# Kernel tuning notes

Hardware: AMD Instinct MI355X
Metric: run time of the kernel (lower is better)

The kernel has to match this reference:

```python
import jax, jax.numpy as jnp
import numpy as np

N = 50000          # num_nodes
E = 600000         # num_edges
D_IN = 128         # gcn_embed_dims[0]
D_H = 128          # gcn_embed_dims[1]
D_OUT = 64         # gcn_embed_dims[2]
D_MLP = 64         # mlp hidden


def setup_inputs() -> dict:
    key = jax.random.key(0)
    ks = jax.random.split(key, 10)
    s = lambda fan: 1.0 / np.sqrt(fan).astype(np.float32)
    return {
        "X": jax.random.normal(ks[0], (N, D_IN), jnp.float32),
        "edges": jax.random.randint(ks[1], (2, E), 0, N, dtype=jnp.int32),
        # GCN layer 1
        "Wg1": jax.random.normal(ks[2], (D_IN, D_H), jnp.float32) * s(D_IN),
        "bg1": jnp.zeros((D_H,), jnp.float32),
        # GCN layer 2
        "Wg2": jax.random.normal(ks[3], (D_H, D_OUT), jnp.float32) * s(D_H),
        "bg2": jnp.zeros((D_OUT,), jnp.float32),
        # decoder MLP: in = 2*D_OUT = 128
        "Wm1": jax.random.normal(ks[4], (2 * D_OUT, D_MLP), jnp.float32) * s(2 * D_OUT),
        "bm1": jnp.zeros((D_MLP,), jnp.float32),
        "Wm2": jax.random.normal(ks[5], (D_MLP, 1), jnp.float32) * s(D_MLP),
        "bm2": jnp.zeros((1,), jnp.float32),
    }


def gcn_conv(X, W, b, src, dst):
    """GCNConv: out = D^{-1/2} (A + I) D^{-1/2} X W + b (PyG semantics)."""
    n = X.shape[0]
    XW = X @ W                                   # [N, d_out]
    loop = jnp.arange(n, dtype=src.dtype)
    src2 = jnp.concatenate([src, loop])          # add self-loops
    dst2 = jnp.concatenate([dst, loop])
    deg = jax.ops.segment_sum(jnp.ones_like(dst2, dtype=XW.dtype), dst2,
                              num_segments=n)    # in-degree incl. self-loop
    dinv = jax.lax.rsqrt(jnp.maximum(deg, 1.0))  # deg >= 1 due to self-loop
    norm = dinv[src2] * dinv[dst2]               # [E+N]
    out = jax.ops.segment_sum(XW[src2] * norm[:, None], dst2, num_segments=n)
    return out + b


def reference(X, edges, Wg1, bg1, Wg2, bg2, Wm1, bm1, Wm2, bm2):
    src, dst = edges[0], edges[1]
    # encode: GCNConv -> ReLU -> GCNConv
    H = jax.nn.relu(gcn_conv(X, Wg1, bg1, src, dst))
    H = gcn_conv(H, Wg2, bg2, src, dst)          # [N, 64]
    # decode: gather endpoints, concat, MLP
    Z = jnp.concatenate([H[src], H[dst]], axis=-1)  # [E, 128]
    Z = jax.nn.relu(Z @ Wm1 + bm1)                   # [E, 64]
    return Z @ Wm2 + bm2                             # [E, 1]
```

## Files before the change

### kernel.cpp

```cpp
#include <hip/hip_runtime.h>


typedef __attribute__((ext_vector_type(8))) short bf8v;
typedef __attribute__((ext_vector_type(4))) float fa4v;

__device__ __forceinline__ ushort to_bf(float x) {
    unsigned u = __float_as_uint(x);
    unsigned r = (u + 0x7fffu + ((u >> 16) & 1u)) >> 16;
    return (ushort)r;
}
__device__ __forceinline__ float from_bf(ushort h) {
    return __uint_as_float(((unsigned)h) << 16);
}

__global__ void deg_count_k(const int* __restrict__ dst, int* __restrict__ cnt, int E) {
    int i = blockIdx.x * 256 + threadIdx.x;
    if (i < E) atomicAdd(&cnt[dst[i]], 1);
}

__global__ void deg_inv_k(const int* __restrict__ cnt, float* __restrict__ dinv, int n) {
    int i = blockIdx.x * 256 + threadIdx.x;
    if (i < n) dinv[i] = rsqrtf((float)cnt[i] + 1.0f);
}

__global__ void scan_a_k(const int* __restrict__ cnt, int* __restrict__ excl,
                         int* __restrict__ bsum, int n) {
    __shared__ int sd[256];
    int t = threadIdx.x;
    int base = blockIdx.x * 1024 + t * 4;
    int v0 = 0, v1 = 0, v2 = 0, v3 = 0;
    if (base + 0 < n) v0 = cnt[base + 0];
    if (base + 1 < n) v1 = cnt[base + 1];
    if (base + 2 < n) v2 = cnt[base + 2];
    if (base + 3 < n) v3 = cnt[base + 3];
    int sum = v0 + v1 + v2 + v3;
    int acc = sum;
    sd[t] = acc;
    __syncthreads();
    for (int off = 1; off < 256; off <<= 1) {
        int x = (t >= off) ? sd[t - off] : 0;
        __syncthreads();
        acc += x;
        sd[t] = acc;
        __syncthreads();
    }
    int run = acc - sum;
    if (base + 0 < n) excl[base + 0] = run;
    run += v0;
    if (base + 1 < n) excl[base + 1] = run;
    run += v1;
    if (base + 2 < n) excl[base + 2] = run;
    run += v2;
    if (base + 3 < n) excl[base + 3] = run;
    if (t == 255) bsum[blockIdx.x] = acc;
}

__global__ void scan_b_k(int* __restrict__ bsum, int nb) {
    __shared__ int sd[256];
    int t = threadIdx.x;
    int v = (t < nb) ? bsum[t] : 0;
    int acc = v;
    sd[t] = acc;
    __syncthreads();
    for (int off = 1; off < 256; off <<= 1) {
        int x = (t >= off) ? sd[t - off] : 0;
        __syncthreads();
        acc += x;
        sd[t] = acc;
        __syncthreads();
    }
    if (t < nb) bsum[t] = acc - v;
}

__global__ void scan_c_k(int* __restrict__ excl, const int* __restrict__ bsum,
                         int* __restrict__ cursor, int n) {
    int i = blockIdx.x * 256 + threadIdx.x;
    if (i < n) {
        int v = excl[i] + bsum[i >> 10];
        excl[i] = v;
        cursor[i] = v;
    }
}

__global__ void csr_fill_k(const int* __restrict__ src, const int* __restrict__ dst,
                           int* __restrict__ cursor, int2* __restrict__ csr_se, int E) {
    int i = blockIdx.x * 256 + threadIdx.x;
    if (i < E) {
        int d = dst[i];
        int p = atomicAdd(&cursor[d], 1);
        int2 se; se.x = src[i]; se.y = i;
        csr_se[p] = se;
    }
}

__global__ void w1t_split_k(const float* __restrict__ W, ushort* __restrict__ Wth,
                            ushort* __restrict__ Wtl) {
    int i = blockIdx.x * 256 + threadIdx.x;
    int n = i >> 7, k = i & 127;
    float x = W[k * 128 + n];
    ushort h = to_bf(x);
    Wth[i] = h;
    Wtl[i] = to_bf(x - from_bf(h));
}

__global__ void wfold_split_k(const float* __restrict__ Wg2, const float* __restrict__ bg2,
                              const float* __restrict__ Wm1,
                              ushort* __restrict__ Wfth, ushort* __restrict__ Wftl,
                              float* __restrict__ bcat) {
    int i = blockIdx.x * 256 + threadIdx.x;
    if (i < 128 * 128) {
        int r = i >> 7, c = i & 127;
        const float* wc = (c < 64) ? (Wm1 + c) : (Wm1 + 64 * 64 + (c - 64));
        float acc = 0.f;
#pragma unroll 8
        for (int j = 0; j < 64; ++j) acc = fmaf(Wg2[r * 64 + j], wc[j * 64], acc);
        ushort h = to_bf(acc);
        Wfth[c * 128 + r] = h;
        Wftl[c * 128 + r] = to_bf(acc - from_bf(h));
    } else if (i < 128 * 128 + 128) {
        int c = i - 128 * 128;
        const float* wc = (c < 64) ? (Wm1 + c) : (Wm1 + 64 * 64 + (c - 64));
        float acc = 0.f;
#pragma unroll 8
        for (int j = 0; j < 64; ++j) acc = fmaf(bg2[j], wc[j * 64], acc);
        bcat[c] = acc;
    }
}

__global__ __launch_bounds__(256) void gemm_mfma_k(
    const float* __restrict__ A,
    const ushort* __restrict__ Bth, const ushort* __restrict__ Btl,
    const float* __restrict__ rowscale, ushort* __restrict__ C, int M) {
    __shared__ ushort Bs[2][128][136];
    const int t = threadIdx.x;
#pragma unroll
    for (int i = 0; i < 16; ++i) {
        int c = i * 256 + t;
        int arr = c >> 11;
        int cc = c & 2047;
        int n = cc >> 4, kb = cc & 15;
        const ushort* src = arr ? Btl : Bth;
        bf8v v = *(const bf8v*)(src + n * 128 + kb * 8);
        *(bf8v*)(&Bs[arr][n][kb * 8]) = v;
    }
    __syncthreads();

    const int lane = t & 63;
    const int w = t >> 6;
    const int r16 = lane & 15;
    const int kg = lane >> 4;
    int arow = blockIdx.x * 64 + w * 16 + r16;
    if (arow >= M) arow = M - 1;
    const float* pA = A + (size_t)arow * 128 + kg * 8;

    fa4v acc[8];
#pragma unroll
    for (int ct = 0; ct < 8; ++ct) acc[ct] = (fa4v){0.f, 0.f, 0.f, 0.f};

#pragma unroll
    for (int ks = 0; ks < 4; ++ks) {
        float av[8];
        *(float4*)(&av[0]) = *(const float4*)(pA + ks * 32);
        *(float4*)(&av[4]) = *(const float4*)(pA + ks * 32 + 4);
        bf8v ah, al;
#pragma unroll
        for (int j = 0; j < 8; ++j) {
            ushort h = to_bf(av[j]);
            ah[j] = (short)h;
            al[j] = (short)to_bf(av[j] - from_bf(h));
        }
#pragma unroll
        for (int ct = 0; ct < 8; ++ct) {
            bf8v bh = *(const bf8v*)(&Bs[0][ct * 16 + r16][ks * 32 + kg * 8]);
            bf8v bl = *(const bf8v*)(&Bs[1][ct * 16 + r16][ks * 32 + kg * 8]);
            acc[ct] = __builtin_amdgcn_mfma_f32_16x16x32_bf16(ah, bh, acc[ct], 0, 0, 0);
            acc[ct] = __builtin_amdgcn_mfma_f32_16x16x32_bf16(ah, bl, acc[ct], 0, 0, 0);
            acc[ct] = __builtin_amdgcn_mfma_f32_16x16x32_bf16(al, bh, acc[ct], 0, 0, 0);
        }
    }

    const int rbase = blockIdx.x * 64 + w * 16 + kg * 4;
#pragma unroll
    for (int r = 0; r < 4; ++r) {
        int row = rbase + r;
        if (row < M) {
            float sc = rowscale[row];
#pragma unroll
            for (int ct = 0; ct < 8; ++ct)
                C[(size_t)row * 128 + ct * 16 + r16] = to_bf(acc[ct][r] * sc);
        }
    }
}

template <bool RELU, bool BF16OUT>
__global__ void gcn_agg_k(const ushort* __restrict__ Cb, const float* __restrict__ dinv,
                          const int* __restrict__ row_start, const int* __restrict__ cnt,
                          const int2* __restrict__ csr_se, const float* __restrict__ bias,
                          float* __restrict__ outf, ushort* __restrict__ outh, int n) {
    int wid = (int)((blockIdx.x * blockDim.x + threadIdx.x) >> 6);
    int lane = threadIdx.x & 63;
    if (wid >= n) return;
    float di = dinv[wid];
    int deg = cnt[wid];
    int rs = row_start[wid];
    ushort2 a = *(const ushort2*)(Cb + (size_t)wid * 128 + lane * 2);
    float ax = from_bf(a.x), ay = from_bf(a.y);
    int i = 0;
    while (i < deg) {
        int take = deg - i;
        if (take > 64) take = 64;
        int addr = rs + i + lane;
        int lim = rs + deg - 1;
        if (addr > lim) addr = lim;
        int vidx = csr_se[addr].x;
        int j = 0;
        for (; j + 8 <= take; j += 8) {
            int s0 = __shfl(vidx, j + 0), s1 = __shfl(vidx, j + 1);
            int s2 = __shfl(vidx, j + 2), s3 = __shfl(vidx, j + 3);
            int s4 = __shfl(vidx, j + 4), s5 = __shfl(vidx, j + 5);
            int s6 = __shfl(vidx, j + 6), s7 = __shfl(vidx, j + 7);
            ushort2 u0 = *(const ushort2*)(Cb + (size_t)s0 * 128 + lane * 2);
            ushort2 u1 = *(const ushort2*)(Cb + (size_t)s1 * 128 + lane * 2);
            ushort2 u2 = *(const ushort2*)(Cb + (size_t)s2 * 128 + lane * 2);
            ushort2 u3 = *(const ushort2*)(Cb + (size_t)s3 * 128 + lane * 2);
            ushort2 u4 = *(const ushort2*)(Cb + (size_t)s4 * 128 + lane * 2);
            ushort2 u5 = *(const ushort2*)(Cb + (size_t)s5 * 128 + lane * 2);
            ushort2 u6 = *(const ushort2*)(Cb + (size_t)s6 * 128 + lane * 2);
            ushort2 u7 = *(const ushort2*)(Cb + (size_t)s7 * 128 + lane * 2);
            ax += ((from_bf(u0.x) + from_bf(u1.x)) + (from_bf(u2.x) + from_bf(u3.x))) +
                  ((from_bf(u4.x) + from_bf(u5.x)) + (from_bf(u6.x) + from_bf(u7.x)));
            ay += ((from_bf(u0.y) + from_bf(u1.y)) + (from_bf(u2.y) + from_bf(u3.y))) +
                  ((from_bf(u4.y) + from_bf(u5.y)) + (from_bf(u6.y) + from_bf(u7.y)));
        }
        for (; j + 2 <= take; j += 2) {
            int s0 = __shfl(vidx, j + 0), s1 = __shfl(vidx, j + 1);
            ushort2 u0 = *(const ushort2*)(Cb + (size_t)s0 * 128 + lane * 2);
            ushort2 u1 = *(const ushort2*)(Cb + (size_t)s1 * 128 + lane * 2);
            ax += from_bf(u0.x) + from_bf(u1.x);
            ay += from_bf(u0.y) + from_bf(u1.y);
        }
        if (j < take) {
            int s = __shfl(vidx, j);
            ushort2 u = *(const ushort2*)(Cb + (size_t)s * 128 + lane * 2);
            ax += from_bf(u.x);
            ay += from_bf(u.y);
        }
        i += take;
    }
    float2 b = ((const float2*)bias)[lane];
    ax = fmaf(ax, di, b.x);
    ay = fmaf(ay, di, b.y);
    if constexpr (RELU) {
        ax = fmaxf(ax, 0.f);
        ay = fmaxf(ay, 0.f);
    }
    if constexpr (BF16OUT) {
        ushort2 h;
        h.x = to_bf(ax);
        h.y = to_bf(ay);
        ((ushort2*)outh)[(size_t)wid * 64 + lane] = h;
    } else {
        float2 r; r.x = ax; r.y = ay;
        ((float2*)outf)[(size_t)wid * 64 + lane] = r;
    }
}

__global__ __launch_bounds__(256) void edge_dec_k(
    const ushort* __restrict__ PQ, const int* __restrict__ row_start,
    const int* __restrict__ cnt, const int2* __restrict__ csr_se,
    const float* __restrict__ bm1, const float* __restrict__ w2,
    const float* __restrict__ bm2, float* __restrict__ out, int n) {
    int wid = (int)((blockIdx.x * blockDim.x + threadIdx.x) >> 6);
    int lane = threadIdx.x & 63;
    if (wid >= n) return;
    int deg = cnt[wid];
    if (deg == 0) return;
    int rs = row_start[wid];
    const int sub = lane >> 4;
    const int q = lane & 15;

    const float4 b1v = ((const float4*)bm1)[q];
    const float4 w2v = ((const float4*)w2)[q];
    const float b2 = bm2[0];
    ushort4 Qu = *(const ushort4*)(PQ + (size_t)wid * 128 + 64 + q * 4);
    float4 bq;
    bq.x = from_bf(Qu.x) + b1v.x; bq.y = from_bf(Qu.y) + b1v.y;
    bq.z = from_bf(Qu.z) + b1v.z; bq.w = from_bf(Qu.w) + b1v.w;

    int i = 0;
    while (i < deg) {
        int take = deg - i;
        if (take > 64) take = 64;
        int addr = rs + i + lane;
        int lim = rs + deg - 1;
        if (addr > lim) addr = lim;
        int2 se = csr_se[addr];
        for (int j = 0; j < take; j += 8) {
            int ia = j + sub;
            int ib = j + 4 + sub;
            bool aa = ia < take;
            bool ab = ib < take;
            int sa = __shfl(se.x, aa ? ia : 0);
            int ea = __shfl(se.y, aa ? ia : 0);
            int sb = __shfl(se.x, ab ? ib : 0);
            int eb = __shfl(se.y, ab ? ib : 0);
            ushort4 pua = *(const ushort4*)(PQ + (size_t)sa * 128 + q * 4);
            ushort4 pub = *(const ushort4*)(PQ + (size_t)sb * 128 + q * 4);
            float ha0 = fmaxf(from_bf(pua.x) + bq.x, 0.f);
            float ha1 = fmaxf(from_bf(pua.y) + bq.y, 0.f);
            float ha2 = fmaxf(from_bf(pua.z) + bq.z, 0.f);
            float ha3 = fmaxf(from_bf(pua.w) + bq.w, 0.f);
            float hb0 = fmaxf(from_bf(pub.x) + bq.x, 0.f);
            float hb1 = fmaxf(from_bf(pub.y) + bq.y, 0.f);
            float hb2 = fmaxf(from_bf(pub.z) + bq.z, 0.f);
            float hb3 = fmaxf(from_bf(pub.w) + bq.w, 0.f);
            float va = fmaf(ha0, w2v.x, fmaf(ha1, w2v.y, fmaf(ha2, w2v.z, ha3 * w2v.w)));
            float vb = fmaf(hb0, w2v.x, fmaf(hb1, w2v.y, fmaf(hb2, w2v.z, hb3 * w2v.w)));
            va += __shfl_xor(va, 8, 16);
            va += __shfl_xor(va, 4, 16);
            va += __shfl_xor(va, 2, 16);
            va += __shfl_xor(va, 1, 16);
            vb += __shfl_xor(vb, 8, 16);
            vb += __shfl_xor(vb, 4, 16);
            vb += __shfl_xor(vb, 2, 16);
            vb += __shfl_xor(vb, 1, 16);
            if (aa && q == 0) out[ea] = va + b2;
            if (ab && q == 0) out[eb] = vb + b2;
        }
        i += take;
    }
}


extern "C" void kernel_launch(void* const* d_in, const int* in_sizes, int n_in,
                              void* d_out, int out_size, void* d_ws, size_t ws_size,
                              hipStream_t stream) {
    const float* X   = (const float*)d_in[0];
    const int*  edges = (const int*)d_in[1];
    const float* Wg1 = (const float*)d_in[2];
    const float* bg1 = (const float*)d_in[3];
    const float* Wg2 = (const float*)d_in[4];
    const float* bg2 = (const float*)d_in[5];
    const float* Wm1 = (const float*)d_in[6];
    const float* bm1 = (const float*)d_in[7];
    const float* Wm2 = (const float*)d_in[8];
    const float* bm2 = (const float*)d_in[9];
    float* out = (float*)d_out;

    const int N = in_sizes[0] / 128;
    const int E = in_sizes[1] / 2;
    const int* esrc = edges;
    const int* edst = edges + E;

    char* p = (char*)d_ws;
    auto alloc = [&](size_t nbytes) {
        void* r = (void*)p;
        p += (nbytes + 255) & ~(size_t)255;
        return r;
    };
    float* H      = (float*)alloc((size_t)N * 128 * 4);
    ushort* Cb    = (ushort*)alloc((size_t)N * 128 * 2);
    ushort* PQ    = (ushort*)alloc((size_t)N * 128 * 2);
    float* dinv   = (float*)alloc((size_t)N * 4);
    int* cnt      = (int*)alloc((size_t)N * 4);
    int* rowst    = (int*)alloc((size_t)N * 4);
    int* cursor   = (int*)alloc((size_t)N * 4);
    int* bsum     = (int*)alloc(1024);
    ushort* Wg1th = (ushort*)alloc(128 * 128 * 2);
    ushort* Wg1tl = (ushort*)alloc(128 * 128 * 2);
    ushort* Wfth  = (ushort*)alloc(128 * 128 * 2);
    ushort* Wftl  = (ushort*)alloc(128 * 128 * 2);
    float* bcat   = (float*)alloc(128 * 4);
    int2* csr_se  = (int2*)alloc((size_t)E * 8);
    (void)ws_size; (void)n_in; (void)out_size;

    const int gE = (E + 255) / 256;
    const int gN = (N + 255) / 256;
    const int nb = (N + 1023) / 1024;
    const int gM64 = (N + 63) / 64;
    const int gAgg = (N * 64 + 255) / 256;

    hipMemsetAsync(cnt, 0, (size_t)N * 4, stream);
    deg_count_k<<<gE, 256, 0, stream>>>(edst, cnt, E);
    deg_inv_k<<<gN, 256, 0, stream>>>(cnt, dinv, N);
    scan_a_k<<<nb, 256, 0, stream>>>(cnt, rowst, bsum, N);
    scan_b_k<<<1, 256, 0, stream>>>(bsum, nb);
    scan_c_k<<<gN, 256, 0, stream>>>(rowst, bsum, cursor, N);
    csr_fill_k<<<gE, 256, 0, stream>>>(esrc, edst, cursor, csr_se, E);
    w1t_split_k<<<64, 256, 0, stream>>>(Wg1, Wg1th, Wg1tl);
    wfold_split_k<<<65, 256, 0, stream>>>(Wg2, bg2, Wm1, Wfth, Wftl, bcat);

    gemm_mfma_k<<<gM64, 256, 0, stream>>>(X, Wg1th, Wg1tl, dinv, Cb, N);
    gcn_agg_k<true, false><<<gAgg, 256, 0, stream>>>(Cb, dinv, rowst, cnt, csr_se, bg1,
                                                     H, nullptr, N);
    gemm_mfma_k<<<gM64, 256, 0, stream>>>(H, Wfth, Wftl, dinv, Cb, N);
    gcn_agg_k<false, true><<<gAgg, 256, 0, stream>>>(Cb, dinv, rowst, cnt, csr_se, bcat,
                                                     nullptr, PQ, N);
    edge_dec_k<<<gAgg, 256, 0, stream>>>(PQ, rowst, cnt, csr_se, bm1, Wm2, bm2, out, N);
}
```

Before: 272.4 us.

## Fuse CSR build and weight prep into one cooperative kernel with grid syncs

Replaces the memset plus eight small preprocessing kernels (degree count, inverse degree, three-stage scan, CSR fill, weight splits) with a single cooperative kernel of 1024 blocks that separates the phases with grid.sync(). The scan now uses 256-element blocks and a 1024-entry block-sum array. The aim is to remove per-launch overhead and inter-kernel gaps in the graph-build phase. In exchange it pays for five grid-wide barriers and relies on all 1024 blocks being co-resident, and it hard-codes 1024 blocks, which caps N at 256K for the second-level scan.

```diff
diff --git a/kernel.cpp b/kernel.cpp
--- a/kernel.cpp
+++ b/kernel.cpp
@@ -1,4 +1,7 @@
 #include <hip/hip_runtime.h>
+#include <hip/hip_cooperative_groups.h>
+
+namespace cg = cooperative_groups;
 
 
 typedef __attribute__((ext_vector_type(8))) short bf8v;
@@ -13,117 +16,108 @@
     return __uint_as_float(((unsigned)h) << 16);
 }
 
-__global__ void deg_count_k(const int* __restrict__ dst, int* __restrict__ cnt, int E) {
-    int i = blockIdx.x * 256 + threadIdx.x;
-    if (i < E) atomicAdd(&cnt[dst[i]], 1);
-}
-
-__global__ void deg_inv_k(const int* __restrict__ cnt, float* __restrict__ dinv, int n) {
-    int i = blockIdx.x * 256 + threadIdx.x;
-    if (i < n) dinv[i] = rsqrtf((float)cnt[i] + 1.0f);
-}
-
-__global__ void scan_a_k(const int* __restrict__ cnt, int* __restrict__ excl,
-                         int* __restrict__ bsum, int n) {
-    __shared__ int sd[256];
-    int t = threadIdx.x;
-    int base = blockIdx.x * 1024 + t * 4;
-    int v0 = 0, v1 = 0, v2 = 0, v3 = 0;
-    if (base + 0 < n) v0 = cnt[base + 0];
-    if (base + 1 < n) v1 = cnt[base + 1];
-    if (base + 2 < n) v2 = cnt[base + 2];
-    if (base + 3 < n) v3 = cnt[base + 3];
-    int sum = v0 + v1 + v2 + v3;
-    int acc = sum;
-    sd[t] = acc;
-    __syncthreads();
-    for (int off = 1; off < 256; off <<= 1) {
-        int x = (t >= off) ? sd[t - off] : 0;
+__global__ __launch_bounds__(256) void build_k(
+    const int* __restrict__ esrc, const int* __restrict__ edst,
+    int* __restrict__ cnt, float* __restrict__ dinv, int* __restrict__ rowst,
+    int* __restrict__ cursor, int* __restrict__ bsum, int2* __restrict__ csr_se,
+    const float* __restrict__ Wg1, const float* __restrict__ Wg2,
+    const float* __restrict__ bg2, const float* __restrict__ Wm1,
+    ushort* __restrict__ Wg1th, ushort* __restrict__ Wg1tl,
+    ushort* __restrict__ Wfth, ushort* __restrict__ Wftl, float* __restrict__ bcat,
+    int N, int E) {
+    cg::grid_group grid = cg::this_grid();
+    __shared__ int sh[256];
+    const int tid = (int)(blockIdx.x * 256 + threadIdx.x);
+    const int nt = (int)(gridDim.x * 256);
+
+    for (int i = tid; i < N; i += nt) cnt[i] = 0;
+    if (tid < 128 * 128) {
+        int n = tid >> 7, k = tid & 127;
+        float x = Wg1[k * 128 + n];
+        ushort h = to_bf(x);
+        Wg1th[tid] = h;
+        Wg1tl[tid] = to_bf(x - from_bf(h));
+    }
+    {
+        int j = tid - 128 * 128;
+        if (j >= 0 && j < 128 * 128) {
+            int r = j >> 7, c = j & 127;
+            const float* wc = (c < 64) ? (Wm1 + c) : (Wm1 + 64 * 64 + (c - 64));
+            float acc = 0.f;
+#pragma unroll 8
+            for (int q = 0; q < 64; ++q) acc = fmaf(Wg2[r * 64 + q], wc[q * 64], acc);
+            ushort h = to_bf(acc);
+            Wfth[c * 128 + r] = h;
+            Wftl[c * 128 + r] = to_bf(acc - from_bf(h));
+        } else if (j >= 128 * 128 && j < 128 * 128 + 128) {
+            int c = j - 128 * 128;
+            const float* wc = (c < 64) ? (Wm1 + c) : (Wm1 + 64 * 64 + (c - 64));
+            float acc = 0.f;
+#pragma unroll 8
+            for (int q = 0; q < 64; ++q) acc = fmaf(bg2[q], wc[q * 64], acc);
+            bcat[c] = acc;
+        }
+    }
+    grid.sync();
+
+    for (int i = tid; i < E; i += nt) atomicAdd(&cnt[edst[i]], 1);
+    grid.sync();
+
+    {
+        int base = (int)blockIdx.x * 256;
+        int idx = base + (int)threadIdx.x;
+        int v = (idx < N) ? cnt[idx] : 0;
+        int acc = v;
+        sh[threadIdx.x] = acc;
         __syncthreads();
-        acc += x;
-        sd[t] = acc;
+        for (int off = 1; off < 256; off <<= 1) {
+            int x = ((int)threadIdx.x >= off) ? sh[threadIdx.x - off] : 0;
+            __syncthreads();
+            acc += x;
+            sh[threadIdx.x] = acc;
+            __syncthreads();
+        }
+        if (idx < N) rowst[idx] = acc - v;
+        if (threadIdx.x == 255) bsum[blockIdx.x] = (base < N) ? acc : 0;
+    }
+    grid.sync();
+
+    if (blockIdx.x == 0) {
+        int t = (int)threadIdx.x;
+        int v0 = bsum[t * 4 + 0], v1 = bsum[t * 4 + 1];
+        int v2 = bsum[t * 4 + 2], v3 = bsum[t * 4 + 3];
+        int sum = v0 + v1 + v2 + v3;
+        int acc = sum;
+        sh[t] = acc;
         __syncthreads();
-    }
-    int run = acc - sum;
-    if (base + 0 < n) excl[base + 0] = run;
-    run += v0;
-    if (base + 1 < n) excl[base + 1] = run;
-    run += v1;
-    if (base + 2 < n) excl[base + 2] = run;
-    run += v2;
-    if (base + 3 < n) excl[base + 3] = run;
-    if (t == 255) bsum[blockIdx.x] = acc;
-}
-
-__global__ void scan_b_k(int* __restrict__ bsum, int nb) {
-    __shared__ int sd[256];
-    int t = threadIdx.x;
-    int v = (t < nb) ? bsum[t] : 0;
-    int acc = v;
-    sd[t] = acc;
-    __syncthreads();
-    for (int off = 1; off < 256; off <<= 1) {
-        int x = (t >= off) ? sd[t - off] : 0;
-        __syncthreads();
-        acc += x;
-        sd[t] = acc;
-        __syncthreads();
-    }
-    if (t < nb) bsum[t] = acc - v;
-}
-
-__global__ void scan_c_k(int* __restrict__ excl, const int* __restrict__ bsum,
-                         int* __restrict__ cursor, int n) {
-    int i = blockIdx.x * 256 + threadIdx.x;
-    if (i < n) {
-        int v = excl[i] + bsum[i >> 10];
-        excl[i] = v;
+        for (int off = 1; off < 256; off <<= 1) {
+            int x = (t >= off) ? sh[t - off] : 0;
+            __syncthreads();
+            acc += x;
+            sh[t] = acc;
+            __syncthreads();
+        }
+        int run = acc - sum;
+        bsum[t * 4 + 0] = run; run += v0;
+        bsum[t * 4 + 1] = run; run += v1;
+        bsum[t * 4 + 2] = run; run += v2;
+        bsum[t * 4 + 3] = run;
+    }
+    grid.sync();
+
+    for (int i = tid; i < N; i += nt) {
+        int v = rowst[i] + bsum[i >> 8];
+        rowst[i] = v;
         cursor[i] = v;
-    }
-}
-
-__global__ void csr_fill_k(const int* __restrict__ src, const int* __restrict__ dst,
-                           int* __restrict__ cursor, int2* __restrict__ csr_se, int E) {
-    int i = blockIdx.x * 256 + threadIdx.x;
-    if (i < E) {
-        int d = dst[i];
+        dinv[i] = rsqrtf((float)cnt[i] + 1.0f);
+    }
+    grid.sync();
+
+    for (int i = tid; i < E; i += nt) {
+        int d = edst[i];
         int p = atomicAdd(&cursor[d], 1);
-        int2 se; se.x = src[i]; se.y = i;
+        int2 se; se.x = esrc[i]; se.y = i;
         csr_se[p] = se;
-    }
-}
-
-__global__ void w1t_split_k(const float* __restrict__ W, ushort* __restrict__ Wth,
-                            ushort* __restrict__ Wtl) {
-    int i = blockIdx.x * 256 + threadIdx.x;
-    int n = i >> 7, k = i & 127;
-    float x = W[k * 128 + n];
-    ushort h = to_bf(x);
-    Wth[i] = h;
-    Wtl[i] = to_bf(x - from_bf(h));
-}
-
-__global__ void wfold_split_k(const float* __restrict__ Wg2, const float* __restrict__ bg2,
-                              const float* __restrict__ Wm1,
-                              ushort* __restrict__ Wfth, ushort* __restrict__ Wftl,
-                              float* __restrict__ bcat) {
-    int i = blockIdx.x * 256 + threadIdx.x;
-    if (i < 128 * 128) {
-        int r = i >> 7, c = i & 127;
-        const float* wc = (c < 64) ? (Wm1 + c) : (Wm1 + 64 * 64 + (c - 64));
-        float acc = 0.f;
-#pragma unroll 8
-        for (int j = 0; j < 64; ++j) acc = fmaf(Wg2[r * 64 + j], wc[j * 64], acc);
-        ushort h = to_bf(acc);
-        Wfth[c * 128 + r] = h;
-        Wftl[c * 128 + r] = to_bf(acc - from_bf(h));
-    } else if (i < 128 * 128 + 128) {
-        int c = i - 128 * 128;
-        const float* wc = (c < 64) ? (Wm1 + c) : (Wm1 + 64 * 64 + (c - 64));
-        float acc = 0.f;
-#pragma unroll 8
-        for (int j = 0; j < 64; ++j) acc = fmaf(bg2[j], wc[j * 64], acc);
-        bcat[c] = acc;
     }
 }
 
@@ -365,7 +359,7 @@
     int* cnt      = (int*)alloc((size_t)N * 4);
     int* rowst    = (int*)alloc((size_t)N * 4);
     int* cursor   = (int*)alloc((size_t)N * 4);
-    int* bsum     = (int*)alloc(1024);
+    int* bsum     = (int*)alloc(4096);
     ushort* Wg1th = (ushort*)alloc(128 * 128 * 2);
     ushort* Wg1tl = (ushort*)alloc(128 * 128 * 2);
     ushort* Wfth  = (ushort*)alloc(128 * 128 * 2);
@@ -374,21 +368,19 @@
     int2* csr_se  = (int2*)alloc((size_t)E * 8);
     (void)ws_size; (void)n_in; (void)out_size;
 
-    const int gE = (E + 255) / 256;
-    const int gN = (N + 255) / 256;
-    const int nb = (N + 1023) / 1024;
     const int gM64 = (N + 63) / 64;
     const int gAgg = (N * 64 + 255) / 256;
 
-    hipMemsetAsync(cnt, 0, (size_t)N * 4, stream);
-    deg_count_k<<<gE, 256, 0, stream>>>(edst, cnt, E);
-    deg_inv_k<<<gN, 256, 0, stream>>>(cnt, dinv, N);
-    scan_a_k<<<nb, 256, 0, stream>>>(cnt, rowst, bsum, N);
-    scan_b_k<<<1, 256, 0, stream>>>(bsum, nb);
-    scan_c_k<<<gN, 256, 0, stream>>>(rowst, bsum, cursor, N);
-    csr_fill_k<<<gE, 256, 0, stream>>>(esrc, edst, cursor, csr_se, E);
-    w1t_split_k<<<64, 256, 0, stream>>>(Wg1, Wg1th, Wg1tl);
-    wfold_split_k<<<65, 256, 0, stream>>>(Wg2, bg2, Wm1, Wfth, Wftl, bcat);
+    {
+        void* ka[] = {
+            (void*)&esrc, (void*)&edst, (void*)&cnt, (void*)&dinv, (void*)&rowst,
+            (void*)&cursor, (void*)&bsum, (void*)&csr_se,
+            (void*)&Wg1, (void*)&Wg2, (void*)&bg2, (void*)&Wm1,
+            (void*)&Wg1th, (void*)&Wg1tl, (void*)&Wfth, (void*)&Wftl, (void*)&bcat,
+            (void*)&N, (void*)&E,
+        };
+        hipLaunchCooperativeKernel((void*)build_k, dim3(1024), dim3(256), ka, 0, stream);
+    }
 
     gemm_mfma_k<<<gM64, 256, 0, stream>>>(X, Wg1th, Wg1tl, dinv, Cb, N);
     gcn_agg_k<true, false><<<gAgg, 256, 0, stream>>>(Cb, dinv, rowst, cnt, csr_se, bg1,
```

Result: slower. 766.9 us (+181.6%).
